# Performance work log

Measured on AMD Instinct MI355X. Metric: run time of the kernel, lower is better.

Reference implementation:

```python
import jax, jax.numpy as jnp
import numpy as np

IN_CH = 64
OUT_CH = 64
SEQ_LEN = 2048
MODES = 64  # modes2 = min(modes1, seq_len//2) = 64
SCALE = 1.0 / (IN_CH * OUT_CH)


def setup_inputs() -> dict:
    key = jax.random.key(0)
    k1, k2, k3 = jax.random.split(key, 3)
    x = jax.random.normal(k1, (32, 8, IN_CH, SEQ_LEN), dtype=jnp.float32)
    # torch.rand(...) complex init scaled by 1/(in*out): real & imag in [0, scale)
    wr = SCALE * jax.random.uniform(k2, (IN_CH, OUT_CH, MODES), dtype=jnp.float32)
    wi = SCALE * jax.random.uniform(k3, (IN_CH, OUT_CH, MODES), dtype=jnp.float32)
    return {"x": x, "wr": wr, "wi": wi}


def reference(x, wr, wi):
    # x: [B, H, E, N] real; weights complex [in, out, modes]
    N = x.shape[-1]
    w = jax.lax.complex(wr, wi)
    x_ft = jnp.fft.rfft(x)                       # [B, H, E, N//2+1] complex64
    a = x_ft[..., :MODES]                        # keep only low modes
    out_low = jnp.einsum('bjix,iox->bjox', a, w)  # per-mode complex matmul
    # zero-fill remaining frequency bins (equivalent to out_ft zeros + slice set)
    pad = N // 2 + 1 - MODES
    out_ft = jnp.pad(out_low, ((0, 0), (0, 0), (0, 0), (0, pad)))
    return jnp.fft.irfft(out_ft, n=N)            # [B, H, out_ch, N] real
```

## Files before the change

### kernel.cpp

```cpp
#include <hip/hip_runtime.h>
#include <hip/hip_bf16.h>


typedef __bf16 bf16x8 __attribute__((ext_vector_type(8)));
typedef float  f32x4  __attribute__((ext_vector_type(4)));

#define SEQ 2048
#define NM2 128
#define KS  4
#define TWO_PI_OVER_N 3.0679615757712823e-03f

__device__ __forceinline__ unsigned int rnbf(float f) {
  unsigned int u = __builtin_bit_cast(unsigned int, f);
  return (u + 0x7fffu + ((u >> 16) & 1u)) >> 16;
}
__device__ __forceinline__ unsigned int pack2(float a, float b) {
  return rnbf(a) | (rnbf(b) << 16);
}
__device__ __forceinline__ float frombf(unsigned int lo16_in_place) {
  return __builtin_bit_cast(float, lo16_in_place);
}

typedef const __attribute__((address_space(1))) unsigned int gu32;
typedef __attribute__((address_space(3))) unsigned int lu32;

__global__ __launch_bounds__(256) void k_tables(unsigned short* __restrict__ t1sw,
                                                unsigned short* __restrict__ t2t) {
  int idx = blockIdx.x * 256 + threadIdx.x;
  int c = idx >> 11;
  int n = idx & 2047;
  int k = c & 63;
  float ph = (float)((k * n) & 2047) * TWO_PI_OVER_N;
  float s, co;
  sincosf(ph, &s, &co);
  float v1 = (c < 64) ? co : -s;
  float ck = (k == 0 ? 1.0f : 2.0f) * (1.0f / 2048.0f);
  float v2 = (c < 64) ? ck * co : -ck * s;
  int kt = n >> 6, part = (n >> 3) & 7, e = n & 7;
  unsigned off = (unsigned)kt * 16384u +
                 (((unsigned)(c * 128 + part * 16)) ^ (((unsigned)c & 7u) << 4)) + 2u * (unsigned)e;
  *(unsigned short*)((char*)t1sw + off) = (unsigned short)rnbf(v1);
  t2t[n * NM2 + c] = (unsigned short)rnbf(v2);
}

__global__ __launch_bounds__(256) void k_gemm1(const float* __restrict__ x,
                                               const unsigned short* __restrict__ t1sw,
                                               unsigned short* __restrict__ P) {
  __shared__ int4 lds4[49152 / 16];
  char* lds = (char*)lds4;
  const int tid = threadIdx.x;
  const int wave = tid >> 6, lane = tid & 63;
  const int mtile = blockIdx.x >> 2, ks = blockIdx.x & (KS - 1);
  const int r0 = mtile * 64;
  const int kbase = ks * (SEQ / KS);

  f32x4 acc[8] = {};

  const int row_s = tid >> 2;
  const int q_s = tid & 3;
  const float* xrow = x + (size_t)(r0 + row_s) * SEQ + kbase + q_s * 16;
  const unsigned xorA = (unsigned)(row_s & 7) << 4;
  const unsigned sA0 = ((unsigned)(row_s * 128 + q_s * 32)) ^ xorA;
  const unsigned sA1 = ((unsigned)(row_s * 128 + q_s * 32 + 16)) ^ xorA;

  const char* t1base = (const char*)t1sw + (size_t)(kbase >> 6) * 16384;

  f32x4 f[4];
#pragma unroll
  for (int m = 0; m < 4; ++m) f[m] = *(const f32x4*)(xrow + m * 4);
#pragma unroll
  for (int p = 0; p < 4; ++p) {
    __builtin_amdgcn_global_load_lds((gu32*)(t1base + (p * 256 + tid) * 16),
                                     (lu32*)(lds + 16384 + (p * 256 + wave * 64) * 16),
                                     16, 0, 0);
  }
  {
    unsigned pk[8];
#pragma unroll
    for (int m = 0; m < 4; ++m) {
      pk[2 * m]     = pack2(f[m][0], f[m][1]);
      pk[2 * m + 1] = pack2(f[m][2], f[m][3]);
    }
    uint4 w0; w0.x = pk[0]; w0.y = pk[1]; w0.z = pk[2]; w0.w = pk[3];
    uint4 w1; w1.x = pk[4]; w1.y = pk[5]; w1.z = pk[6]; w1.w = pk[7];
    *(uint4*)(lds + sA0) = w0;
    *(uint4*)(lds + sA1) = w1;
  }
  __syncthreads();

  for (int it = 0; it < 8; ++it) {
    const int cur = it & 1, nxt = cur ^ 1;
    const int xoff = cur * 8192;
    const int toff = 16384 + cur * 16384;
    if (it < 7) {
      const char* tg = t1base + (it + 1) * 16384;
#pragma unroll
      for (int p = 0; p < 4; ++p) {
        __builtin_amdgcn_global_load_lds((gu32*)(tg + (p * 256 + tid) * 16),
                                         (lu32*)(lds + 16384 + nxt * 16384 + (p * 256 + wave * 64) * 16),
                                         16, 0, 0);
      }
#pragma unroll
      for (int m = 0; m < 4; ++m) f[m] = *(const f32x4*)(xrow + (it + 1) * 64 + m * 4);
    }
#pragma unroll
    for (int kss = 0; kss < 2; ++kss) {
      const int arow = wave * 16 + (lane & 15);
      const bf16x8 av = *(const bf16x8*)(lds + xoff +
          ((arow * 128 + kss * 64 + ((lane >> 4) * 16)) ^ ((unsigned)(arow & 7) << 4)));
#pragma unroll
      for (int t = 0; t < 8; ++t) {
        const int col = t * 16 + (lane & 15);
        const bf16x8 bv = *(const bf16x8*)(lds + toff +
            ((col * 128 + kss * 64 + ((lane >> 4) * 16)) ^ ((unsigned)(col & 7) << 4)));
        acc[t] = __builtin_amdgcn_mfma_f32_16x16x32_bf16(av, bv, acc[t], 0, 0, 0);
      }
    }
    if (it < 7) {
      unsigned pk[8];
#pragma unroll
      for (int m = 0; m < 4; ++m) {
        pk[2 * m]     = pack2(f[m][0], f[m][1]);
        pk[2 * m + 1] = pack2(f[m][2], f[m][3]);
      }
      uint4 w0; w0.x = pk[0]; w0.y = pk[1]; w0.z = pk[2]; w0.w = pk[3];
      uint4 w1; w1.x = pk[4]; w1.y = pk[5]; w1.z = pk[6]; w1.w = pk[7];
      *(uint4*)(lds + nxt * 8192 + sA0) = w0;
      *(uint4*)(lds + nxt * 8192 + sA1) = w1;
    }
    __syncthreads();
  }
  unsigned short* Pout = P + (size_t)ks * (16384 * NM2);
#pragma unroll
  for (int t = 0; t < 8; ++t) {
    const int col = t * 16 + (lane & 15);
#pragma unroll
    for (int j = 0; j < 4; ++j) {
      const int row = r0 + wave * 16 + (lane >> 4) * 4 + j;
      Pout[row * NM2 + col] = (unsigned short)rnbf(acc[t][j]);
    }
  }
}

__global__ __launch_bounds__(256) void k_stage2(const unsigned short* __restrict__ P,
                                                const float* __restrict__ wr,
                                                const float* __restrict__ wi,
                                                unsigned short* __restrict__ Bx) {
  __shared__ float sA[4][64][64];
  const int b = blockIdx.x;
  const int bjc = b >> 2, oh = (b >> 1) & 1, kh = b & 1;
  const int k0 = kh * 32;
  const int tid = threadIdx.x;
#pragma unroll
  for (int p = 0; p < 16; ++p) {
    int fidx = tid + 256 * p;
    int row_lin = fidx >> 4, q = fidx & 15;
    int col = (q < 8) ? (k0 + q * 4) : (64 + k0 + (q - 8) * 4);
    const unsigned short* base = P + (size_t)(bjc * 256 + row_lin) * NM2 + col;
    f32x4 v = {};
#pragma unroll
    for (int s = 0; s < KS; ++s) {
      uint2 u = *(const uint2*)(base + (size_t)s * (16384 * NM2));
      v[0] += frombf(u.x << 16);
      v[1] += frombf(u.x & 0xffff0000u);
      v[2] += frombf(u.y << 16);
      v[3] += frombf(u.y & 0xffff0000u);
    }
    *(f32x4*)(&sA[row_lin >> 6][row_lin & 63][q * 4]) = v;
  }
  __syncthreads();
  const int o_l = tid >> 3, kg = tid & 7;
  const int o = oh * 32 + o_l;
  const int kb = k0 + kg * 4;
  f32x4 accr[4] = {};
  f32x4 acci[4] = {};
  for (int i = 0; i < 64; ++i) {
    f32x4 wrv = *(const f32x4*)(wr + (i * 64 + o) * 64 + kb);
    f32x4 wiv = *(const f32x4*)(wi + (i * 64 + o) * 64 + kb);
#pragma unroll
    for (int bj = 0; bj < 4; ++bj) {
      f32x4 ar = *(const f32x4*)(&sA[bj][i][kg * 4]);
      f32x4 ai = *(const f32x4*)(&sA[bj][i][32 + kg * 4]);
#pragma unroll
      for (int kk = 0; kk < 4; ++kk) {
        accr[bj][kk] += ar[kk] * wrv[kk] - ai[kk] * wiv[kk];
        acci[bj][kk] += ar[kk] * wiv[kk] + ai[kk] * wrv[kk];
      }
    }
  }
#pragma unroll
  for (int bj = 0; bj < 4; ++bj) {
    const int r = (bjc * 4 + bj) * 64 + o;
    uint2 vr; vr.x = pack2(accr[bj][0], accr[bj][1]); vr.y = pack2(accr[bj][2], accr[bj][3]);
    uint2 vi; vi.x = pack2(acci[bj][0], acci[bj][1]); vi.y = pack2(acci[bj][2], acci[bj][3]);
    *(uint2*)(Bx + r * NM2 + kb)      = vr;
    *(uint2*)(Bx + r * NM2 + 64 + kb) = vi;
  }
}

__global__ __launch_bounds__(256) void k_gemm2(const unsigned short* __restrict__ Bx,
                                               const unsigned short* __restrict__ t2t,
                                               float* __restrict__ out) {
  __shared__ int4 lds4[65536 / 16];
  char* lds = (char*)lds4;
  const int tid = threadIdx.x, wave = tid >> 6, lane = tid & 63;
  const int mb = blockIdx.x >> 4, nb = blockIdx.x & 15;
  const int r0 = mb * 128, n0 = nb * 128;
#pragma unroll
  for (int p = 0; p < 8; ++p) {
    int seg = tid + 256 * p;
    int row = seg >> 4, part = seg & 15;
    unsigned sw = (unsigned)((row * 256 + part * 16) ^ ((row & 7) << 4));
    int4 va = *(const int4*)(Bx + (r0 + row) * NM2 + part * 8);
    *(int4*)(lds + sw) = va;
    int4 vb = *(const int4*)(t2t + (n0 + row) * NM2 + part * 8);
    *(int4*)(lds + 32768 + sw) = vb;
  }
  __syncthreads();
  f32x4 acc[2][8] = {};
#pragma unroll
  for (int ks = 0; ks < 4; ++ks) {
    const int ar0 = wave * 32 + (lane & 15);
    const int ar1 = ar0 + 16;
    const int koff = ks * 64 + (lane >> 4) * 16;
    bf16x8 a0 = *(const bf16x8*)(lds + ((ar0 * 256 + koff) ^ ((unsigned)(ar0 & 7) << 4)));
    bf16x8 a1 = *(const bf16x8*)(lds + ((ar1 * 256 + koff) ^ ((unsigned)(ar1 & 7) << 4)));
#pragma unroll
    for (int t = 0; t < 8; ++t) {
      const int col = t * 16 + (lane & 15);
      bf16x8 bv = *(const bf16x8*)(lds + 32768 + ((col * 256 + koff) ^ ((unsigned)(col & 7) << 4)));
      acc[0][t] = __builtin_amdgcn_mfma_f32_16x16x32_bf16(a0, bv, acc[0][t], 0, 0, 0);
      acc[1][t] = __builtin_amdgcn_mfma_f32_16x16x32_bf16(a1, bv, acc[1][t], 0, 0, 0);
    }
  }
#pragma unroll
  for (int m = 0; m < 2; ++m) {
#pragma unroll
    for (int t = 0; t < 8; ++t) {
      const int col = n0 + t * 16 + (lane & 15);
#pragma unroll
      for (int j = 0; j < 4; ++j) {
        const int row = r0 + wave * 32 + m * 16 + (lane >> 4) * 4 + j;
        out[row * SEQ + col] = acc[m][t][j];
      }
    }
  }
}

extern "C" void kernel_launch(void* const* d_in, const int* in_sizes, int n_in,
                              void* d_out, int out_size, void* d_ws, size_t ws_size,
                              hipStream_t stream) {
  const float* x  = (const float*)d_in[0];
  const float* wr = (const float*)d_in[1];
  const float* wi = (const float*)d_in[2];
  float* out = (float*)d_out;
  char* ws = (char*)d_ws;
  unsigned short* t1sw = (unsigned short*)(ws);
  unsigned short* t2t  = (unsigned short*)(ws + 524288);
  unsigned short* P    = (unsigned short*)(ws + 1048576);
  unsigned short* Bx   = (unsigned short*)(ws + 1048576 + (size_t)KS * 16384 * NM2 * 2);

  k_tables<<<dim3(1024), dim3(256), 0, stream>>>(t1sw, t2t);
  k_gemm1 <<<dim3(256 * KS), dim3(256), 0, stream>>>(x, t1sw, P);
  k_stage2<<<dim3(256),  dim3(256), 0, stream>>>(P, wr, wi, Bx);
  k_gemm2 <<<dim3(2048), dim3(256), 0, stream>>>(Bx, t2t, out);
}
```

Before: 103.8 us.

## Stream fp32 x tiles into LDS asynchronously and convert at fragment load

gemm1 now loads the fp32 input tiles straight into LDS with global_load_lds, using an XOR-swizzled layout, instead of going through registers and packing to bf16 before an LDS store. The bf16 conversion moves to the A-fragment read via v_cvt_pk_bf16_f32. The K split drops from 4 to 2, which doubles the loop length and halves the partial-sum traffic. gemm2 also remaps block indices for L2 locality and reorders the store loops. In exchange, LDS use per block rises to 64KB, the fp32 tiles double LDS bandwidth per tile, and the smaller K split halves the number of gemm1 blocks, which can hurt occupancy.

New measurement: 89.93 us. -13.4%, faster.

```diff
diff --git a/kernel.cpp b/kernel.cpp
--- a/kernel.cpp
+++ b/kernel.cpp
@@ -7,7 +7,7 @@
 
 #define SEQ 2048
 #define NM2 128
-#define KS  4
+#define KS  2
 #define TWO_PI_OVER_N 3.0679615757712823e-03f
 
 __device__ __forceinline__ unsigned int rnbf(float f) {
@@ -46,89 +46,78 @@
 __global__ __launch_bounds__(256) void k_gemm1(const float* __restrict__ x,
                                                const unsigned short* __restrict__ t1sw,
                                                unsigned short* __restrict__ P) {
-  __shared__ int4 lds4[49152 / 16];
+  __shared__ int4 lds4[65536 / 16];
   char* lds = (char*)lds4;
-  const int tid = threadIdx.x;
-  const int wave = tid >> 6, lane = tid & 63;
-  const int mtile = blockIdx.x >> 2, ks = blockIdx.x & (KS - 1);
+  const int tid = threadIdx.x, wave = tid >> 6, lane = tid & 63;
+  const int mtile = blockIdx.x >> 1, ks = blockIdx.x & (KS - 1);
   const int r0 = mtile * 64;
   const int kbase = ks * (SEQ / KS);
+  const char* t1base = (const char*)t1sw + (size_t)(kbase >> 6) * 16384;
+
+  const float* xsrc[4];
+#pragma unroll
+  for (int p = 0; p < 4; ++p) {
+    const int row = p * 16 + wave * 4 + (lane >> 4);
+    const int u = (lane & 15) ^ (row & 7);
+    xsrc[p] = x + (size_t)(r0 + row) * SEQ + kbase + u * 4;
+  }
 
   f32x4 acc[8] = {};
 
-  const int row_s = tid >> 2;
-  const int q_s = tid & 3;
-  const float* xrow = x + (size_t)(r0 + row_s) * SEQ + kbase + q_s * 16;
-  const unsigned xorA = (unsigned)(row_s & 7) << 4;
-  const unsigned sA0 = ((unsigned)(row_s * 128 + q_s * 32)) ^ xorA;
-  const unsigned sA1 = ((unsigned)(row_s * 128 + q_s * 32 + 16)) ^ xorA;
-
-  const char* t1base = (const char*)t1sw + (size_t)(kbase >> 6) * 16384;
-
-  f32x4 f[4];
-#pragma unroll
-  for (int m = 0; m < 4; ++m) f[m] = *(const f32x4*)(xrow + m * 4);
-#pragma unroll
-  for (int p = 0; p < 4; ++p) {
+#pragma unroll
+  for (int p = 0; p < 4; ++p)
+    __builtin_amdgcn_global_load_lds((gu32*)(xsrc[p]),
+                                     (lu32*)(lds + p * 4096 + wave * 1024), 16, 0, 0);
+#pragma unroll
+  for (int p = 0; p < 4; ++p)
     __builtin_amdgcn_global_load_lds((gu32*)(t1base + (p * 256 + tid) * 16),
-                                     (lu32*)(lds + 16384 + (p * 256 + wave * 64) * 16),
-                                     16, 0, 0);
-  }
-  {
-    unsigned pk[8];
-#pragma unroll
-    for (int m = 0; m < 4; ++m) {
-      pk[2 * m]     = pack2(f[m][0], f[m][1]);
-      pk[2 * m + 1] = pack2(f[m][2], f[m][3]);
-    }
-    uint4 w0; w0.x = pk[0]; w0.y = pk[1]; w0.z = pk[2]; w0.w = pk[3];
-    uint4 w1; w1.x = pk[4]; w1.y = pk[5]; w1.z = pk[6]; w1.w = pk[7];
-    *(uint4*)(lds + sA0) = w0;
-    *(uint4*)(lds + sA1) = w1;
-  }
-  __syncthreads();
-
-  for (int it = 0; it < 8; ++it) {
+                                     (lu32*)(lds + 32768 + (p * 256 + wave * 64) * 16), 16, 0, 0);
+  asm volatile("s_waitcnt vmcnt(0)" ::: "memory");
+  __builtin_amdgcn_s_barrier();
+
+  const int a = wave * 16 + (lane & 15);
+  const unsigned xra = (unsigned)(a & 7) << 4;
+  const int kg = lane >> 4;
+
+  for (int it = 0; it < 16; ++it) {
     const int cur = it & 1, nxt = cur ^ 1;
-    const int xoff = cur * 8192;
-    const int toff = 16384 + cur * 16384;
-    if (it < 7) {
+    const int xoff = cur * 16384;
+    const int toff = 32768 + cur * 16384;
+    if (it < 15) {
       const char* tg = t1base + (it + 1) * 16384;
 #pragma unroll
-      for (int p = 0; p < 4; ++p) {
+      for (int p = 0; p < 4; ++p)
+        __builtin_amdgcn_global_load_lds((gu32*)(xsrc[p] + (it + 1) * 64),
+                                         (lu32*)(lds + nxt * 16384 + p * 4096 + wave * 1024),
+                                         16, 0, 0);
+#pragma unroll
+      for (int p = 0; p < 4; ++p)
         __builtin_amdgcn_global_load_lds((gu32*)(tg + (p * 256 + tid) * 16),
-                                         (lu32*)(lds + 16384 + nxt * 16384 + (p * 256 + wave * 64) * 16),
+                                         (lu32*)(lds + 32768 + nxt * 16384 + (p * 256 + wave * 64) * 16),
                                          16, 0, 0);
-      }
-#pragma unroll
-      for (int m = 0; m < 4; ++m) f[m] = *(const f32x4*)(xrow + (it + 1) * 64 + m * 4);
     }
 #pragma unroll
     for (int kss = 0; kss < 2; ++kss) {
-      const int arow = wave * 16 + (lane & 15);
-      const bf16x8 av = *(const bf16x8*)(lds + xoff +
-          ((arow * 128 + kss * 64 + ((lane >> 4) * 16)) ^ ((unsigned)(arow & 7) << 4)));
+      const unsigned byte0 = (unsigned)(a * 256 + kss * 128 + kg * 32);
+      const f32x4 lo = *(const f32x4*)(lds + xoff + (byte0 ^ xra));
+      const f32x4 hi = *(const f32x4*)(lds + xoff + ((byte0 + 16) ^ xra));
+      unsigned c0, c1, c2, c3;
+      asm("v_cvt_pk_bf16_f32 %0, %1, %2" : "=v"(c0) : "v"(lo[0]), "v"(lo[1]));
+      asm("v_cvt_pk_bf16_f32 %0, %1, %2" : "=v"(c1) : "v"(lo[2]), "v"(lo[3]));
+      asm("v_cvt_pk_bf16_f32 %0, %1, %2" : "=v"(c2) : "v"(hi[0]), "v"(hi[1]));
+      asm("v_cvt_pk_bf16_f32 %0, %1, %2" : "=v"(c3) : "v"(hi[2]), "v"(hi[3]));
+      uint4 pk; pk.x = c0; pk.y = c1; pk.z = c2; pk.w = c3;
+      const bf16x8 av = __builtin_bit_cast(bf16x8, pk);
 #pragma unroll
       for (int t = 0; t < 8; ++t) {
         const int col = t * 16 + (lane & 15);
         const bf16x8 bv = *(const bf16x8*)(lds + toff +
-            ((col * 128 + kss * 64 + ((lane >> 4) * 16)) ^ ((unsigned)(col & 7) << 4)));
+            ((col * 128 + kss * 64 + kg * 16) ^ ((unsigned)(col & 7) << 4)));
         acc[t] = __builtin_amdgcn_mfma_f32_16x16x32_bf16(av, bv, acc[t], 0, 0, 0);
       }
     }
-    if (it < 7) {
-      unsigned pk[8];
-#pragma unroll
-      for (int m = 0; m < 4; ++m) {
-        pk[2 * m]     = pack2(f[m][0], f[m][1]);
-        pk[2 * m + 1] = pack2(f[m][2], f[m][3]);
-      }
-      uint4 w0; w0.x = pk[0]; w0.y = pk[1]; w0.z = pk[2]; w0.w = pk[3];
-      uint4 w1; w1.x = pk[4]; w1.y = pk[5]; w1.z = pk[6]; w1.w = pk[7];
-      *(uint4*)(lds + nxt * 8192 + sA0) = w0;
-      *(uint4*)(lds + nxt * 8192 + sA1) = w1;
-    }
-    __syncthreads();
+    asm volatile("s_waitcnt vmcnt(0)" ::: "memory");
+    __builtin_amdgcn_s_barrier();
   }
   unsigned short* Pout = P + (size_t)ks * (16384 * NM2);
 #pragma unroll
@@ -204,7 +193,8 @@
   __shared__ int4 lds4[65536 / 16];
   char* lds = (char*)lds4;
   const int tid = threadIdx.x, wave = tid >> 6, lane = tid & 63;
-  const int mb = blockIdx.x >> 4, nb = blockIdx.x & 15;
+  const int swz = (blockIdx.x & 7) * 256 + (blockIdx.x >> 3);
+  const int mb = swz >> 4, nb = swz & 15;
   const int r0 = mb * 128, n0 = nb * 128;
 #pragma unroll
   for (int p = 0; p < 8; ++p) {
@@ -236,11 +226,11 @@
 #pragma unroll
   for (int m = 0; m < 2; ++m) {
 #pragma unroll
-    for (int t = 0; t < 8; ++t) {
-      const int col = n0 + t * 16 + (lane & 15);
-#pragma unroll
-      for (int j = 0; j < 4; ++j) {
-        const int row = r0 + wave * 32 + m * 16 + (lane >> 4) * 4 + j;
+    for (int j = 0; j < 4; ++j) {
+      const int row = r0 + wave * 32 + m * 16 + (lane >> 4) * 4 + j;
+#pragma unroll
+      for (int t = 0; t < 8; ++t) {
+        const int col = n0 + t * 16 + (lane & 15);
         out[row * SEQ + col] = acc[m][t][j];
       }
     }
```
